# Kernel optimization log

Measured on AMD Instinct MI355X. Metric: run time of the kernel, lower is better.

Reference implementation:

```python
import jax, jax.numpy as jnp
import numpy as np

EPS = 1.0
TAU = 10.0
STRIDE = 1

def setup_inputs() -> dict:
    key = jax.random.key(0)
    k1, k2 = jax.random.split(key)
    x = jax.random.normal(k1, (8, 8, 2048), dtype=jnp.float32)        # (b, m, T)
    weights = jax.random.normal(k2, (32, 8, 32), dtype=jnp.float32)   # (n, m, l)
    return {"x": x, "weights": weights}

def reference(x, weights):
    n, m, l = weights.shape
    b, _, T = x.shape
    t = (T - l) // STRIDE + 1
    # unfold: (b, m, t, l) windows
    idx = jnp.arange(t)[:, None] * STRIDE + jnp.arange(l)[None, :]
    xw = x[:, :, idx]                                   # (b, m, t, l)
    # euclidean distance via norm expansion (avoids (b,t,n,m,l) blowup):
    # ||x_w - w||^2 = ||x_w||^2 + ||w||^2 - 2 x_w . w
    x2 = (xw * xw).sum(-1).transpose(0, 2, 1)           # (b, t, m)
    w2 = (weights * weights).sum(-1)                    # (n, m)
    dot = jnp.einsum('bmtl,nml->btnm', xw, weights)     # (b, t, n, m)
    d2 = x2[:, :, None, :] + w2[None, None, :, :] - 2.0 * dot
    d = jnp.sqrt(jnp.clip(d2, 0.0))                     # (b, t, n, m)
    # lse pooling over time axis t
    logits_t = -(EPS * d) ** 2
    pooled = jax.nn.logsumexp(TAU * logits_t, axis=1) / TAU   # (b, n, m)
    pred = jnp.exp(pooled)
    d_min = d.min(axis=1)                               # (b, n, m)
    return pred.reshape(b, -1), d_min.reshape(b, -1)
```

## Files before the change

### kernel.cpp

```cpp
#include <hip/hip_runtime.h>
#include <math.h>


#define T_VALID 2017
#define K10 14.426950408889634f
#define BIG 1e30f

typedef __attribute__((ext_vector_type(8))) short bf16x8;
typedef __attribute__((ext_vector_type(4))) float f32x4;

union FragU { unsigned u[4]; uint4 q; bf16x8 v; };

__device__ __forceinline__ float fexp2(float v) {
    float r; asm("v_exp_f32 %0, %1" : "=v"(r) : "v"(v)); return r;
}
__device__ __forceinline__ unsigned cvtpk(float lo, float hi) {
    unsigned r; asm("v_cvt_pk_bf16_f32 %0, %1, %2" : "=v"(r) : "v"(lo), "v"(hi)); return r;
}

__global__ __launch_bounds__(512)
__attribute__((amdgpu_waves_per_eu(2, 2)))
void shapelet_mfma(
    const float* __restrict__ x,
    const float* __restrict__ w,
    float* __restrict__ out)
{
    __shared__ unsigned xs8[8 * 257 * 4];
    __shared__ float ssl[2048];
    __shared__ float red[8][16];
    __shared__ float gml[16];

    const int bid = blockIdx.x;
    const int b = bid >> 4;
    const int m = (bid >> 1) & 7;
    const int ntile = bid & 1;
    const int tid = threadIdx.x;
    const int lane = tid & 63;
    const int wv = tid >> 6;
    const int r = lane & 15;
    const int q = lane >> 4;

    const float* xr = x + (((b << 3) + m) << 11);

    const int n = (ntile << 4) + r;
    const float* wrow = w + (((n << 3) + m) << 5);
    const float4 f0 = ((const float4*)wrow)[(q << 1)];
    const float4 f1 = ((const float4*)wrow)[(q << 1) + 1];

    {
        const float4* x4g = (const float4*)xr;
        float xs[36];
        #pragma unroll
        for (int jj = 0; jj < 9; ++jj) {
            int idx = tid + jj;
            idx = idx > 511 ? 511 : idx;
            const float4 v = x4g[idx];
            xs[4 * jj + 0] = v.x; xs[4 * jj + 1] = v.y;
            xs[4 * jj + 2] = v.z; xs[4 * jj + 3] = v.w;
        }
        #pragma unroll
        for (int k = 0; k < 4; ++k) {
            const int p = (tid << 2) + k;
            FragU ch;
            ch.u[0] = cvtpk(xs[k + 0], xs[k + 1]);
            ch.u[1] = cvtpk(xs[k + 2], xs[k + 3]);
            ch.u[2] = cvtpk(xs[k + 4], xs[k + 5]);
            ch.u[3] = cvtpk(xs[k + 6], xs[k + 7]);
            *(uint4*)&xs8[((p & 7) * 257 + (p >> 3)) << 2] = ch.q;
        }
        float sv0 = 0.0f;
        #pragma unroll
        for (int l = 0; l < 32; ++l) sv0 = fmaf(xs[l], xs[l], sv0);
        float sv[4];
        sv[0] = sv0;
        #pragma unroll
        for (int i = 1; i < 4; ++i)
            sv[i] = fmaf(xs[31 + i], xs[31 + i], sv[i - 1]) - xs[i - 1] * xs[i - 1];
        const int t0 = tid << 2;
        #pragma unroll
        for (int i = 0; i < 4; ++i)
            if (t0 + i >= T_VALID) sv[i] = BIG;
        f32x4 s4 = {sv[0], sv[1], sv[2], sv[3]};
        *(f32x4*)&ssl[t0] = s4;
    }

    FragU bf;
    bf.u[0] = cvtpk(f0.x, f0.y); bf.u[1] = cvtpk(f0.z, f0.w);
    bf.u[2] = cvtpk(f1.x, f1.y); bf.u[3] = cvtpk(f1.z, f1.w);
    float w2v = f0.x * f0.x;
    w2v = fmaf(f0.y, f0.y, w2v); w2v = fmaf(f0.z, f0.z, w2v);
    w2v = fmaf(f0.w, f0.w, w2v); w2v = fmaf(f1.x, f1.x, w2v);
    w2v = fmaf(f1.y, f1.y, w2v); w2v = fmaf(f1.z, f1.z, w2v);
    w2v = fmaf(f1.w, f1.w, w2v);
    w2v += __shfl_xor(w2v, 16);
    w2v += __shfl_xor(w2v, 32);

    __syncthreads();

    float dA[64];
    #pragma unroll
    for (int i = 0; i < 16; ++i) {
        const int tt = (wv << 4) + i;
        int b0 = (tt << 4) + r + (q << 3);
        b0 = b0 > 2040 ? 2040 : b0;
        FragU af;
        af.q = *(const uint4*)&xs8[((b0 & 7) * 257 + (b0 >> 3)) << 2];
        f32x4 z = {0.0f, 0.0f, 0.0f, 0.0f};
        const f32x4 acc = __builtin_amdgcn_mfma_f32_16x16x32_bf16(af.v, bf.v, z, 0, 0, 0);
        const f32x4 sv = *(const f32x4*)&ssl[(tt << 4) + (q << 2)];
        dA[4 * i + 0] = fmaf(-2.0f, acc[0], sv[0] + w2v);
        dA[4 * i + 1] = fmaf(-2.0f, acc[1], sv[1] + w2v);
        dA[4 * i + 2] = fmaf(-2.0f, acc[2], sv[2] + w2v);
        dA[4 * i + 3] = fmaf(-2.0f, acc[3], sv[3] + w2v);
    }

    float m0 = dA[0];
    #pragma unroll
    for (int k = 1; k < 64; ++k) m0 = fminf(m0, dA[k]);
    m0 = fminf(m0, __shfl_xor(m0, 16));
    m0 = fminf(m0, __shfl_xor(m0, 32));
    if (lane < 16) red[wv][r] = m0;
    __syncthreads();
    if (tid < 16) {
        float g = red[0][tid];
        #pragma unroll
        for (int wq = 1; wq < 8; ++wq) g = fminf(g, red[wq][tid]);
        gml[tid] = g;
    }
    __syncthreads();

    const float g0 = gml[r];
    float sa0 = 0.0f, sa1 = 0.0f, sa2 = 0.0f, sa3 = 0.0f;
    #pragma unroll
    for (int k = 0; k < 64; k += 4) {
        sa0 += fexp2(K10 * (g0 - dA[k + 0]));
        sa1 += fexp2(K10 * (g0 - dA[k + 1]));
        sa2 += fexp2(K10 * (g0 - dA[k + 2]));
        sa3 += fexp2(K10 * (g0 - dA[k + 3]));
    }
    float S = (sa0 + sa1) + (sa2 + sa3);
    S += __shfl_xor(S, 16);
    S += __shfl_xor(S, 32);
    if (lane < 16) red[wv][r] = S;
    __syncthreads();

    if (tid < 16) {
        float Ssum = red[0][tid];
        #pragma unroll
        for (int wq = 1; wq < 8; ++wq) Ssum += red[wq][tid];
        const float g = gml[tid];
        const int o = (b << 8) + (((ntile << 4) + tid) << 3) + m;
        out[o]        = expf(-g + 0.1f * logf(Ssum));
        out[2048 + o] = sqrtf(fmaxf(g, 0.0f));
    }
}

extern "C" void kernel_launch(void* const* d_in, const int* in_sizes, int n_in,
                              void* d_out, int out_size, void* d_ws, size_t ws_size,
                              hipStream_t stream) {
    const float* x = (const float*)d_in[0];
    const float* w = (const float*)d_in[1];
    float* out = (float*)d_out;
    hipLaunchKernelGGL(shapelet_mfma, dim3(128), dim3(512), 0, stream, x, w, out);
}
```

Before: 10.02 us.

## Replace block barrier with per-wave LDS wait by duplicating halo conversion

Each wave now converts the extra halo chunks of x that its MFMA windows overlap into the next wave's region, so every wave only reads shared data it wrote itself. That lets the first __syncthreads be replaced by an lgkmcnt wait plus a scheduling barrier, removing a block-wide stall. The squared-norm accumulation is also split into four independent chains to shorten the dependency chain. The cost is a few redundant global loads and conversions, plus reliance on the exact per-wave index footprint staying correct.

Measured after the change: 10.99 us. +9.7%, slower.

```diff
diff --git a/kernel.cpp b/kernel.cpp
--- a/kernel.cpp
+++ b/kernel.cpp
@@ -41,6 +41,7 @@
     const int q = lane >> 4;
 
     const float* xr = x + (((b << 3) + m) << 11);
+    const float4* x4g = (const float4*)xr;
 
     const int n = (ntile << 4) + r;
     const float* wrow = w + (((n << 3) + m) << 5);
@@ -48,7 +49,6 @@
     const float4 f1 = ((const float4*)wrow)[(q << 1) + 1];
 
     {
-        const float4* x4g = (const float4*)xr;
         float xs[36];
         #pragma unroll
         for (int jj = 0; jj < 9; ++jj) {
@@ -68,11 +68,16 @@
             ch.u[3] = cvtpk(xs[k + 6], xs[k + 7]);
             *(uint4*)&xs8[((p & 7) * 257 + (p >> 3)) << 2] = ch.q;
         }
-        float sv0 = 0.0f;
+        float c0 = 0.0f, c1 = 0.0f, c2 = 0.0f, c3 = 0.0f;
         #pragma unroll
-        for (int l = 0; l < 32; ++l) sv0 = fmaf(xs[l], xs[l], sv0);
+        for (int l = 0; l < 32; l += 4) {
+            c0 = fmaf(xs[l + 0], xs[l + 0], c0);
+            c1 = fmaf(xs[l + 1], xs[l + 1], c1);
+            c2 = fmaf(xs[l + 2], xs[l + 2], c2);
+            c3 = fmaf(xs[l + 3], xs[l + 3], c3);
+        }
         float sv[4];
-        sv[0] = sv0;
+        sv[0] = (c0 + c1) + (c2 + c3);
         #pragma unroll
         for (int i = 1; i < 4; ++i)
             sv[i] = fmaf(xs[31 + i], xs[31 + i], sv[i - 1]) - xs[i - 1] * xs[i - 1];
@@ -82,6 +87,26 @@
             if (t0 + i >= T_VALID) sv[i] = BIG;
         f32x4 s4 = {sv[0], sv[1], sv[2], sv[3]};
         *(f32x4*)&ssl[t0] = s4;
+    }
+
+    if (wv < 7 && lane < 6) {
+        const int p0 = (wv << 8) + 256 + (lane << 2);
+        const float4 v0 = x4g[(p0 >> 2) + 0];
+        const float4 v1 = x4g[(p0 >> 2) + 1];
+        const float4 v2 = x4g[(p0 >> 2) + 2];
+        float ys[12] = {v0.x, v0.y, v0.z, v0.w,
+                        v1.x, v1.y, v1.z, v1.w,
+                        v2.x, v2.y, v2.z, v2.w};
+        #pragma unroll
+        for (int k = 0; k < 4; ++k) {
+            const int p = p0 + k;
+            FragU ch;
+            ch.u[0] = cvtpk(ys[k + 0], ys[k + 1]);
+            ch.u[1] = cvtpk(ys[k + 2], ys[k + 3]);
+            ch.u[2] = cvtpk(ys[k + 4], ys[k + 5]);
+            ch.u[3] = cvtpk(ys[k + 6], ys[k + 7]);
+            *(uint4*)&xs8[((p & 7) * 257 + (p >> 3)) << 2] = ch.q;
+        }
     }
 
     FragU bf;
@@ -95,7 +120,8 @@
     w2v += __shfl_xor(w2v, 16);
     w2v += __shfl_xor(w2v, 32);
 
-    __syncthreads();
+    asm volatile("s_waitcnt lgkmcnt(0)" ::: "memory");
+    __builtin_amdgcn_sched_barrier(0);
 
     float dA[64];
     #pragma unroll
```
